# Optimization experiments

Hardware: AMD Instinct MI355X
Metric: run time of the kernel (lower is better)

Reference implementation:

```python
import jax, jax.numpy as jnp
import numpy as np

D_MODEL = 1024
NHEAD = 16
HEAD_DIM = D_MODEL // NHEAD
D_FF = 4096
EPS = 1e-5


def _layernorm(x, g, b):
    mu = jnp.mean(x, axis=-1, keepdims=True)
    var = jnp.mean((x - mu) ** 2, axis=-1, keepdims=True)
    return (x - mu) * jax.lax.rsqrt(var + EPS) * g + b


def setup_inputs() -> dict:
    key = jax.random.key(0)
    ks = jax.random.split(key, 13)
    s = 1.0 / np.sqrt(D_MODEL)
    sf = 1.0 / np.sqrt(D_FF)
    # weights stored as [in, out] (transposed torch Linear)
    return {
        "src": jax.random.normal(ks[0], (4, 2048, D_MODEL), jnp.float32),
        "Wq": jax.random.uniform(ks[1], (D_MODEL, D_MODEL), jnp.float32, -s, s),
        "bq": jnp.zeros((D_MODEL,), jnp.float32),
        "Wk": jax.random.uniform(ks[2], (D_MODEL, D_MODEL), jnp.float32, -s, s),
        "bk": jnp.zeros((D_MODEL,), jnp.float32),
        "Wv": jax.random.uniform(ks[3], (D_MODEL, D_MODEL), jnp.float32, -s, s),
        "bv": jnp.zeros((D_MODEL,), jnp.float32),
        "Wo": jax.random.uniform(ks[4], (D_MODEL, D_MODEL), jnp.float32, -s, s),
        "bo": jnp.zeros((D_MODEL,), jnp.float32),
        "W1": jax.random.uniform(ks[5], (D_MODEL, D_FF), jnp.float32, -s, s),
        "b1": jnp.zeros((D_FF,), jnp.float32),
        "W2": jax.random.uniform(ks[6], (D_FF, D_MODEL), jnp.float32, -sf, sf),
        "b2": jnp.zeros((D_MODEL,), jnp.float32),
        "g1": jnp.ones((D_MODEL,), jnp.float32),
        "be1": jnp.zeros((D_MODEL,), jnp.float32),
        "g2": jnp.ones((D_MODEL,), jnp.float32),
        "be2": jnp.zeros((D_MODEL,), jnp.float32),
    }


def reference(src, Wq, bq, Wk, bk, Wv, bv, Wo, bo, W1, b1, W2, b2, g1, be1, g2, be2):
    B, S, _ = src.shape
    scale = 1.0 / np.sqrt(HEAD_DIM)
    # project and split heads: [B, H, S, Dh]
    def heads(W, b):
        return (src @ W + b).reshape(B, S, NHEAD, HEAD_DIM).transpose(0, 2, 1, 3)
    Q, K, V = heads(Wq, bq), heads(Wk, bk), heads(Wv, bv)
    scores = jnp.einsum('bhqd,bhkd->bhqk', Q, K) * scale
    attn = jax.nn.softmax(scores, axis=-1)
    ctx = jnp.einsum('bhqk,bhkd->bhqd', attn, V)
    ctx = ctx.transpose(0, 2, 1, 3).reshape(B, S, D_MODEL)
    attn_out = ctx @ Wo + bo
    x = _layernorm(src + attn_out, g1, be1)
    ff = jax.nn.relu(x @ W1 + b1) @ W2 + b2
    return _layernorm(x + ff, g2, be2)
```

## Files before the change

kernel.cpp:

```cpp
#include <hip/hip_runtime.h>

typedef __attribute__((ext_vector_type(8))) short bf16x8;
typedef __attribute__((ext_vector_type(4))) float f32x4;
typedef unsigned short u16;
typedef unsigned int u32;

__device__ __forceinline__ u16 f2b(float f) {
  u32 u = __float_as_uint(f);
  u = (u + 0x7fffu + ((u >> 16) & 1u)) >> 16;
  return (u16)u;
}
__device__ __forceinline__ float b2f(u16 b) {
  return __uint_as_float(((u32)b) << 16);
}
__device__ __forceinline__ u32 cvtpk_bf16(float lo, float hi) {
  u32 r;
  asm("v_cvt_pk_bf16_f32 %0, %1, %2" : "=v"(r) : "v"(lo), "v"(hi));
  return r;
}
__device__ __forceinline__ void gload_lds16(const u16* g, u16* l) {
  __builtin_amdgcn_global_load_lds(
      (const __attribute__((address_space(1))) void*)g,
      (__attribute__((address_space(3))) void*)l, 16, 0, 0);
}

__global__ __launch_bounds__(256) void cvt_bf16(const float* __restrict__ in,
                                                u16* __restrict__ out, int n4) {
  int i = blockIdx.x * 256 + threadIdx.x;
  if (i >= n4) return;
  float4 v = ((const float4*)in)[i];
  ushort4 o;
  o.x = f2b(v.x); o.y = f2b(v.y); o.z = f2b(v.z); o.w = f2b(v.w);
  ((ushort4*)out)[i] = o;
}

__global__ __launch_bounds__(256) void transpose_w(const float* __restrict__ in,
                                                   u16* __restrict__ out,
                                                   int R, int C) {
  __shared__ float t[32][33];
  int tid = threadIdx.x, tx = tid & 31, ty = tid >> 5;
  int rb = blockIdx.y * 32, cb = blockIdx.x * 32;
  for (int i = 0; i < 4; i++)
    t[ty + i * 8][tx] = in[(size_t)(rb + ty + i * 8) * C + cb + tx];
  __syncthreads();
  for (int i = 0; i < 4; i++)
    out[(size_t)(cb + ty + i * 8) * R + rb + tx] = f2b(t[tx][ty + i * 8]);
}

__global__ __launch_bounds__(256) void concat3(const float* __restrict__ a,
                                               const float* __restrict__ b,
                                               const float* __restrict__ c,
                                               float* __restrict__ o) {
  int i = blockIdx.x * 256 + threadIdx.x;
  if (i >= 3072) return;
  o[i] = i < 1024 ? a[i] : (i < 2048 ? b[i - 1024] : c[i - 2048]);
}

__device__ __forceinline__ void stage_quarter(const u16* __restrict__ src,
                                              size_t rowbase, int K, int kcol,
                                              u16* dst, int c, int srow, int sg,
                                              int wid) {
  int row_ = c * 64 + srow;
  int gs_ = sg ^ (row_ & 7);
  gload_lds16(src + (rowbase + row_) * K + kcol + gs_ * 8,
              &dst[(c * 64 + wid * 8) * 64]);
}

template <bool PF>
__device__ __forceinline__ void tile_step(
    const u16* sAc, const u16* sBc, u16* sAn, u16* sBn,
    const u16* __restrict__ A, const u16* __restrict__ Bt, size_t abase,
    size_t bbase, int K, int Tn, int wm, int wn, int l16, int lq, int srow,
    int sg, int wid, f32x4 (&acc)[8][4]) {
  __syncthreads();
#pragma unroll
  for (int ks = 0; ks < 2; ++ks) {
    bf16x8 Bf[4], Af[4];
#pragma unroll
    for (int j = 0; j < 4; ++j) {
      int r = wn * 64 + j * 16 + l16;
      Bf[j] = *(const bf16x8*)&sBc[r * 64 + (((ks * 4 + lq) ^ (r & 7)) << 3)];
    }
#pragma unroll
    for (int i = 0; i < 4; ++i) {
      int r = wm * 128 + i * 16 + l16;
      Af[i] = *(const bf16x8*)&sAc[r * 64 + (((ks * 4 + lq) ^ (r & 7)) << 3)];
    }
    if (PF) {
      const u16* src = (ks == 0) ? A : Bt;
      size_t rb = (ks == 0) ? abase : bbase;
      u16* dst = (ks == 0) ? sAn : sBn;
      stage_quarter(src, rb, K, Tn * 64, dst, 0, srow, sg, wid);
      stage_quarter(src, rb, K, Tn * 64, dst, 1, srow, sg, wid);
    }
    __builtin_amdgcn_s_setprio(1);
#pragma unroll
    for (int i = 0; i < 4; ++i)
#pragma unroll
      for (int j = 0; j < 4; ++j)
        acc[i][j] = __builtin_amdgcn_mfma_f32_16x16x32_bf16(Af[i], Bf[j],
                                                            acc[i][j], 0, 0, 0);
    __builtin_amdgcn_s_setprio(0);
#pragma unroll
    for (int i = 0; i < 4; ++i) {
      int r = wm * 128 + 64 + i * 16 + l16;
      Af[i] = *(const bf16x8*)&sAc[r * 64 + (((ks * 4 + lq) ^ (r & 7)) << 3)];
    }
    if (PF) {
      const u16* src = (ks == 0) ? A : Bt;
      size_t rb = (ks == 0) ? abase : bbase;
      u16* dst = (ks == 0) ? sAn : sBn;
      stage_quarter(src, rb, K, Tn * 64, dst, 2, srow, sg, wid);
      stage_quarter(src, rb, K, Tn * 64, dst, 3, srow, sg, wid);
    }
    __builtin_amdgcn_s_setprio(1);
#pragma unroll
    for (int i = 0; i < 4; ++i)
#pragma unroll
      for (int j = 0; j < 4; ++j)
        acc[4 + i][j] = __builtin_amdgcn_mfma_f32_16x16x32_bf16(
            Af[i], Bf[j], acc[4 + i][j], 0, 0, 0);
    __builtin_amdgcn_s_setprio(0);
  }
}

template <int MODE>
__global__ __launch_bounds__(512, 1) void gemm256(const u16* __restrict__ A,
                                                  const u16* __restrict__ Bt,
                                                  const float* __restrict__ bias,
                                                  void* __restrict__ out,
                                                  int M, int N, int K,
                                                  float oscale) {
  __shared__ u16 sA0[256 * 64];
  __shared__ u16 sB0[256 * 64];
  __shared__ u16 sA1[256 * 64];
  __shared__ u16 sB1[256 * 64];
  const int tid = threadIdx.x, lane = tid & 63, wid = tid >> 6;
  const int l16 = lane & 15, lq = lane >> 4;
  const int wm = wid >> 2, wn = wid & 3;
  const size_t abase = (size_t)blockIdx.x * 256;
  const size_t bbase = (size_t)blockIdx.y * 256;
  const int srow = tid >> 3;
  const int sg = tid & 7;
  const int nt = K >> 6;

  f32x4 acc[8][4];
#pragma unroll
  for (int i = 0; i < 8; ++i)
#pragma unroll
    for (int j = 0; j < 4; ++j) acc[i][j] = (f32x4){0.f, 0.f, 0.f, 0.f};

#pragma unroll
  for (int c = 0; c < 4; ++c) {
    stage_quarter(A, abase, K, 0, sA0, c, srow, sg, wid);
    stage_quarter(Bt, bbase, K, 0, sB0, c, srow, sg, wid);
  }

  int T = 0;
  for (; T + 2 < nt; T += 2) {
    tile_step<true>(sA0, sB0, sA1, sB1, A, Bt, abase, bbase, K, T + 1, wm, wn,
                    l16, lq, srow, sg, wid, acc);
    tile_step<true>(sA1, sB1, sA0, sB0, A, Bt, abase, bbase, K, T + 2, wm, wn,
                    l16, lq, srow, sg, wid, acc);
  }
  tile_step<true>(sA0, sB0, sA1, sB1, A, Bt, abase, bbase, K, nt - 1, wm, wn,
                  l16, lq, srow, sg, wid, acc);
  tile_step<false>(sA1, sB1, sA0, sB0, A, Bt, abase, bbase, K, 0, wm, wn, l16,
                   lq, srow, sg, wid, acc);

  const int gmb = blockIdx.x * 256 + wm * 128;
  const int gnb = blockIdx.y * 256 + wn * 64;
#pragma unroll
  for (int i = 0; i < 8; ++i) {
    int gm0 = gmb + i * 16 + lq * 4;
#pragma unroll
    for (int j = 0; j < 4; ++j) {
      int gn = gnb + j * 16 + l16;
      float bv = bias[gn];
#pragma unroll
      for (int r = 0; r < 4; ++r) {
        float v = acc[i][j][r] + bv;
        ((u16*)out)[(size_t)(gm0 + r) * N + gn] = f2b(v > 0.f ? v : 0.f);
      }
    }
  }
}

template <bool PF>
__device__ __forceinline__ void tile_stepR(
    const u16* sAc, const u16* sBc, u16* sAn, u16* sBn,
    const u16* __restrict__ A, const u16* __restrict__ Bt, size_t abase,
    size_t bbase, int K, int Tn, int wm, int wn, int l16, int lq, int srow,
    int sg, int wid, f32x4 (&acc)[4][4]) {
  __syncthreads();
#pragma unroll
  for (int ks = 0; ks < 2; ++ks) {
    bf16x8 Bf[4], Af[4];
#pragma unroll
    for (int j = 0; j < 4; ++j) {
      int r = wn * 64 + j * 16 + l16;
      Bf[j] = *(const bf16x8*)&sBc[r * 64 + (((ks * 4 + lq) ^ (r & 7)) << 3)];
    }
#pragma unroll
    for (int i = 0; i < 4; ++i) {
      int r = wm * 64 + i * 16 + l16;
      Af[i] = *(const bf16x8*)&sAc[r * 64 + (((ks * 4 + lq) ^ (r & 7)) << 3)];
    }
    if (PF) {
      if (ks == 0) {
        stage_quarter(A, abase, K, Tn * 64, sAn, 0, srow, sg, wid);
        stage_quarter(A, abase, K, Tn * 64, sAn, 1, srow, sg, wid);
        stage_quarter(Bt, bbase, K, Tn * 64, sBn, 0, srow, sg, wid);
      } else {
        stage_quarter(Bt, bbase, K, Tn * 64, sBn, 1, srow, sg, wid);
        stage_quarter(Bt, bbase, K, Tn * 64, sBn, 2, srow, sg, wid);
        stage_quarter(Bt, bbase, K, Tn * 64, sBn, 3, srow, sg, wid);
      }
    }
    __builtin_amdgcn_s_setprio(1);
#pragma unroll
    for (int i = 0; i < 4; ++i)
#pragma unroll
      for (int j = 0; j < 4; ++j)
        acc[i][j] = __builtin_amdgcn_mfma_f32_16x16x32_bf16(Af[i], Bf[j],
                                                            acc[i][j], 0, 0, 0);
    __builtin_amdgcn_s_setprio(0);
  }
}

template <int MODE>
__global__ __launch_bounds__(512, 1) void gemmR(const u16* __restrict__ A,
                                                const u16* __restrict__ Bt,
                                                const float* __restrict__ bias,
                                                void* __restrict__ out,
                                                int M, int N, int K,
                                                float oscale) {
  __shared__ u16 sA0[128 * 64];
  __shared__ u16 sB0[256 * 64];
  __shared__ u16 sA1[128 * 64];
  __shared__ u16 sB1[256 * 64];
  const int tid = threadIdx.x, lane = tid & 63, wid = tid >> 6;
  const int l16 = lane & 15, lq = lane >> 4;
  const int wm = wid >> 2, wn = wid & 3;
  const size_t abase = (size_t)blockIdx.x * 128;
  const size_t bbase = (size_t)blockIdx.y * 256;
  const int srow = tid >> 3;
  const int sg = tid & 7;
  const int nt = K >> 6;

  f32x4 acc[4][4];
#pragma unroll
  for (int i = 0; i < 4; ++i)
#pragma unroll
    for (int j = 0; j < 4; ++j) acc[i][j] = (f32x4){0.f, 0.f, 0.f, 0.f};

#pragma unroll
  for (int c = 0; c < 2; ++c) stage_quarter(A, abase, K, 0, sA0, c, srow, sg, wid);
#pragma unroll
  for (int c = 0; c < 4; ++c) stage_quarter(Bt, bbase, K, 0, sB0, c, srow, sg, wid);

  int T = 0;
  for (; T + 2 < nt; T += 2) {
    tile_stepR<true>(sA0, sB0, sA1, sB1, A, Bt, abase, bbase, K, T + 1, wm, wn,
                     l16, lq, srow, sg, wid, acc);
    tile_stepR<true>(sA1, sB1, sA0, sB0, A, Bt, abase, bbase, K, T + 2, wm, wn,
                     l16, lq, srow, sg, wid, acc);
  }
  tile_stepR<true>(sA0, sB0, sA1, sB1, A, Bt, abase, bbase, K, nt - 1, wm, wn,
                   l16, lq, srow, sg, wid, acc);
  tile_stepR<false>(sA1, sB1, sA0, sB0, A, Bt, abase, bbase, K, 0, wm, wn, l16,
                    lq, srow, sg, wid, acc);

  const int gmb = blockIdx.x * 128 + wm * 64;
  const int gnb = blockIdx.y * 256 + wn * 64;
#pragma unroll
  for (int i = 0; i < 4; ++i) {
    int gm0 = gmb + i * 16 + lq * 4;
#pragma unroll
    for (int j = 0; j < 4; ++j) {
      int gn = gnb + j * 16 + l16;
      float bv = bias[gn];
      if constexpr (MODE == 1) {
#pragma unroll
        for (int r = 0; r < 4; ++r)
          ((u16*)out)[(size_t)(gm0 + r) * N + gn] = f2b(acc[i][j][r] + bv);
      } else {
        int sel = gn >> 10;
        int h = (gn & 1023) >> 6, d = gn & 63;
        int b = gm0 >> 11, s = gm0 & 2047;
        u16* o = (u16*)out + (size_t)sel * (8u << 20);
        if (sel == 2) {
          ushort4 w;
          w.x = f2b(acc[i][j][0] + bv);
          w.y = f2b(acc[i][j][1] + bv);
          w.z = f2b(acc[i][j][2] + bv);
          w.w = f2b(acc[i][j][3] + bv);
          *(ushort4*)(o + ((size_t)((b * 16 + h) * 64 + d)) * 2048 + s) = w;
        } else {
          float sc = (sel == 0) ? oscale : 1.f;
#pragma unroll
          for (int r = 0; r < 4; ++r)
            o[((size_t)(b * 16 + h) * 2048 + s + r) * 64 + d] =
                f2b((acc[i][j][r] + bv) * sc);
        }
      }
    }
  }
}

__global__ __launch_bounds__(512) void attn_fwd(const u16* __restrict__ Q,
                                                const u16* __restrict__ Kb,
                                                const u16* __restrict__ Vt,
                                                u16* __restrict__ ctx) {
  __shared__ u16 sK[64][64];
  __shared__ u16 sV[64][64];
  __shared__ u16 sP[8][16][72];
  const int tid = threadIdx.x, lane = tid & 63, wid = tid >> 6;
  const int l16 = lane & 15, lq = lane >> 4;
  const int bh = blockIdx.y, qt = blockIdx.x;
  const size_t base = (size_t)bh * (2048 * 64);
  const int xk = l16 & 7;

  bf16x8 qf[2];
  {
    int qrow = qt * 128 + wid * 16 + l16;
    qf[0] = *(const bf16x8*)(Q + base + (size_t)qrow * 64 + lq * 8);
    qf[1] = *(const bf16x8*)(Q + base + (size_t)qrow * 64 + 32 + lq * 8);
  }
  f32x4 o[4];
#pragma unroll
  for (int j = 0; j < 4; j++) o[j] = (f32x4){0.f, 0.f, 0.f, 0.f};
  float lrow = 0.f;

  const int srow = tid >> 3;
  const int sg8 = ((tid & 7) ^ (srow & 7)) * 8;
  const int wslot = (tid & 7) * 8;

  const u16* kp = Kb + base + (size_t)srow * 64 + sg8;
  const u16* vp = Vt + base + (size_t)srow * 2048 + sg8;

  uint4 rk = *(const uint4*)kp;
  uint4 rv = *(const uint4*)vp;

  for (int kv0 = 0; kv0 < 2048; kv0 += 64) {
    __syncthreads();
    *(uint4*)&sK[srow][wslot] = rk;
    *(uint4*)&sV[srow][wslot] = rv;
    if (kv0 + 64 < 2048) {
      int kn = kv0 + 64;
      rk = *(const uint4*)(kp + (size_t)kn * 64);
      rv = *(const uint4*)(vp + kn);
    }
    __syncthreads();

    f32x4 sf[4];
#pragma unroll
    for (int j = 0; j < 4; j++) sf[j] = (f32x4){0.f, 0.f, 0.f, 0.f};
    __builtin_amdgcn_s_setprio(1);
#pragma unroll
    for (int ks = 0; ks < 2; ks++)
#pragma unroll
      for (int j = 0; j < 4; j++) {
        bf16x8 kf = *(const bf16x8*)&sK[j * 16 + l16][((ks * 4 + lq) ^ xk) * 8];
        sf[j] = __builtin_amdgcn_mfma_f32_16x16x32_bf16(kf, qf[ks], sf[j], 0, 0, 0);
      }
    __builtin_amdgcn_s_setprio(0);

    float rs = 0.f;
#pragma unroll
    for (int j = 0; j < 4; j++) {
      float p0 = __builtin_amdgcn_exp2f(sf[j][0]);
      float p1 = __builtin_amdgcn_exp2f(sf[j][1]);
      float p2 = __builtin_amdgcn_exp2f(sf[j][2]);
      float p3 = __builtin_amdgcn_exp2f(sf[j][3]);
      rs += (p0 + p1) + (p2 + p3);
      uint2 w;
      w.x = cvtpk_bf16(p0, p1);
      w.y = cvtpk_bf16(p2, p3);
      *(uint2*)&sP[wid][l16][j * 16 + lq * 4] = w;
    }
    rs += __shfl_xor(rs, 16);
    rs += __shfl_xor(rs, 32);
    lrow += rs;

    __builtin_amdgcn_s_setprio(1);
#pragma unroll
    for (int ks = 0; ks < 2; ks++) {
      bf16x8 pf = *(const bf16x8*)&sP[wid][l16][ks * 32 + lq * 8];
#pragma unroll
      for (int j = 0; j < 4; j++) {
        bf16x8 vf = *(const bf16x8*)&sV[j * 16 + l16][((ks * 4 + lq) ^ xk) * 8];
        o[j] = __builtin_amdgcn_mfma_f32_16x16x32_bf16(pf, vf, o[j], 0, 0, 0);
      }
    }
    __builtin_amdgcn_s_setprio(0);
  }

  float lval[4];
#pragma unroll
  for (int r = 0; r < 4; r++) lval[r] = 1.f / __shfl(lrow, lq * 4 + r);
  const int b = bh >> 4, h = bh & 15;
#pragma unroll
  for (int j = 0; j < 4; j++)
#pragma unroll
    for (int r = 0; r < 4; r++) {
      int srw = qt * 128 + wid * 16 + lq * 4 + r;
      int d = j * 16 + l16;
      ctx[((size_t)(b * 2048 + srw)) * 1024 + h * 64 + d] = f2b(o[j][r] * lval[r]);
    }
}

template <int A_BF16, int B_BF16, int WRITE_F32>
__global__ __launch_bounds__(256) void ln_res(const void* __restrict__ a,
                                              const void* __restrict__ bsrc,
                                              const float* __restrict__ g,
                                              const float* __restrict__ be,
                                              float* __restrict__ outf,
                                              u16* __restrict__ outb) {
  const int row = blockIdx.x, tid = threadIdx.x;
  const size_t off = (size_t)row * 1024 + tid * 4;
  float4 x;
  if constexpr (A_BF16) {
    ushort4 av = *(const ushort4*)((const u16*)a + off);
    x.x = b2f(av.x); x.y = b2f(av.y); x.z = b2f(av.z); x.w = b2f(av.w);
  } else {
    x = *(const float4*)((const float*)a + off);
  }
  if constexpr (B_BF16) {
    ushort4 bv = *(const ushort4*)((const u16*)bsrc + off);
    x.x += b2f(bv.x); x.y += b2f(bv.y); x.z += b2f(bv.z); x.w += b2f(bv.w);
  } else {
    float4 bb = *(const float4*)((const float*)bsrc + off);
    x.x += bb.x; x.y += bb.y; x.z += bb.z; x.w += bb.w;
  }
  float s = x.x + x.y + x.z + x.w;
  float s2 = x.x * x.x + x.y * x.y + x.z * x.z + x.w * x.w;
  for (int o = 1; o < 64; o <<= 1) {
    s += __shfl_xor(s, o);
    s2 += __shfl_xor(s2, o);
  }
  __shared__ float rbuf[8];
  int lane = tid & 63, wid = tid >> 6;
  if (lane == 0) { rbuf[wid] = s; rbuf[4 + wid] = s2; }
  __syncthreads();
  s = rbuf[0] + rbuf[1] + rbuf[2] + rbuf[3];
  s2 = rbuf[4] + rbuf[5] + rbuf[6] + rbuf[7];
  float mu = s * (1.f / 1024.f);
  float var = s2 * (1.f / 1024.f) - mu * mu;
  float rstd = rsqrtf(var + 1e-5f);
  int c = tid * 4;
  float y0 = (x.x - mu) * rstd * g[c + 0] + be[c + 0];
  float y1 = (x.y - mu) * rstd * g[c + 1] + be[c + 1];
  float y2 = (x.z - mu) * rstd * g[c + 2] + be[c + 2];
  float y3 = (x.w - mu) * rstd * g[c + 3] + be[c + 3];
  if constexpr (WRITE_F32) {
    float4 y; y.x = y0; y.y = y1; y.z = y2; y.w = y3;
    *(float4*)(outf + off) = y;
  } else {
    ushort4 yb;
    yb.x = f2b(y0); yb.y = f2b(y1); yb.z = f2b(y2); yb.w = f2b(y3);
    *(ushort4*)(outb + off) = yb;
  }
}

extern "C" void kernel_launch(void* const* d_in, const int* in_sizes, int n_in,
                              void* d_out, int out_size, void* d_ws, size_t ws_size,
                              hipStream_t stream) {
  const float* src = (const float*)d_in[0];
  const float* Wq = (const float*)d_in[1];
  const float* bq = (const float*)d_in[2];
  const float* Wk = (const float*)d_in[3];
  const float* bk = (const float*)d_in[4];
  const float* Wv = (const float*)d_in[5];
  const float* bv = (const float*)d_in[6];
  const float* Wo = (const float*)d_in[7];
  const float* bo = (const float*)d_in[8];
  const float* W1 = (const float*)d_in[9];
  const float* b1 = (const float*)d_in[10];
  const float* W2 = (const float*)d_in[11];
  const float* b2 = (const float*)d_in[12];
  const float* g1 = (const float*)d_in[13];
  const float* be1 = (const float*)d_in[14];
  const float* g2 = (const float*)d_in[15];
  const float* be2 = (const float*)d_in[16];
  float* out = (float*)d_out;
  char* ws = (char*)d_ws;
  const size_t MB = 1ull << 20;

  u16* XB    = (u16*)(ws + 0);
  u16* WQKVT = (u16*)(ws + 16 * MB);
  u16* WOT   = (u16*)(ws + 22 * MB);
  u16* W1T   = (u16*)(ws + 24 * MB);
  u16* W2T   = (u16*)(ws + 32 * MB);
  float* bqkv = (float*)(ws + 40 * MB);
  u16* Qb    = (u16*)(ws + 41 * MB);
  u16* Kbuf  = (u16*)(ws + 57 * MB);
  u16* Vt    = (u16*)(ws + 73 * MB);
  u16* CTX   = XB;
  u16* AO    = (u16*)(ws + 41 * MB);
  u16* H1    = (u16*)(ws + 57 * MB);
  u16* XBUF  = (u16*)(ws + 121 * MB);
  u16* FF    = XB;

  const float QSCALE = 0.125f * 1.44269504088896340736f;

  cvt_bf16<<<dim3(8192), dim3(256), 0, stream>>>(src, XB, 2097152);
  transpose_w<<<dim3(32, 32), dim3(256), 0, stream>>>(Wq, WQKVT, 1024, 1024);
  transpose_w<<<dim3(32, 32), dim3(256), 0, stream>>>(Wk, WQKVT + 1024 * 1024, 1024, 1024);
  transpose_w<<<dim3(32, 32), dim3(256), 0, stream>>>(Wv, WQKVT + 2048 * 1024, 1024, 1024);
  transpose_w<<<dim3(32, 32), dim3(256), 0, stream>>>(Wo, WOT, 1024, 1024);
  transpose_w<<<dim3(128, 32), dim3(256), 0, stream>>>(W1, W1T, 1024, 4096);
  transpose_w<<<dim3(32, 128), dim3(256), 0, stream>>>(W2, W2T, 4096, 1024);
  concat3<<<dim3(12), dim3(256), 0, stream>>>(bq, bk, bv, bqkv);

  gemmR<6><<<dim3(64, 12), dim3(512), 0, stream>>>(XB, WQKVT, bqkv, Qb,
                                                   8192, 3072, 1024, QSCALE);
  attn_fwd<<<dim3(16, 64), dim3(512), 0, stream>>>(Qb, Kbuf, Vt, CTX);
  gemmR<1><<<dim3(64, 4), dim3(512), 0, stream>>>(CTX, WOT, bo, AO,
                                                  8192, 1024, 1024, 1.0f);
  ln_res<0, 1, 0><<<dim3(8192), dim3(256), 0, stream>>>(src, AO, g1, be1, nullptr, XBUF);
  gemm256<2><<<dim3(32, 16), dim3(512), 0, stream>>>(XBUF, W1T, b1, H1,
                                                     8192, 4096, 1024, 1.0f);
  gemmR<1><<<dim3(64, 4), dim3(512), 0, stream>>>(H1, W2T, b2, FF,
                                                  8192, 1024, 4096, 1.0f);
  ln_res<1, 1, 1><<<dim3(8192), dim3(256), 0, stream>>>(XBUF, FF, g2, be2, out, nullptr);
}
```

Baseline: 352.5 us.

## Fuse preprocessing kernels into one launch and defer softmax row-sum shuffles

Merges the input bf16 conversion, the six weight transpose launches and the bias concat into a single prep kernel that dispatches on block index, cutting seven launches and their inter-kernel gaps. The attention kernel also stops reducing the per-row softmax sum across lanes on every key tile. Each lane now accumulates a partial sum and the cross-lane shuffles run once after the loop. The prep kernel now mixes branches with different shared-memory use in one grid, and per-lane partial sums change the floating-point summation order slightly.

```diff
diff --git a/kernel.cpp b/kernel.cpp
--- a/kernel.cpp
+++ b/kernel.cpp
@@ -24,22 +24,12 @@
       (__attribute__((address_space(3))) void*)l, 16, 0, 0);
 }
 
-__global__ __launch_bounds__(256) void cvt_bf16(const float* __restrict__ in,
-                                                u16* __restrict__ out, int n4) {
-  int i = blockIdx.x * 256 + threadIdx.x;
-  if (i >= n4) return;
-  float4 v = ((const float4*)in)[i];
-  ushort4 o;
-  o.x = f2b(v.x); o.y = f2b(v.y); o.z = f2b(v.z); o.w = f2b(v.w);
-  ((ushort4*)out)[i] = o;
-}
-
-__global__ __launch_bounds__(256) void transpose_w(const float* __restrict__ in,
-                                                   u16* __restrict__ out,
-                                                   int R, int C) {
+__device__ __forceinline__ void tr_tile(const float* __restrict__ in,
+                                        u16* __restrict__ out, int R, int C,
+                                        int bx, int by, int tid) {
   __shared__ float t[32][33];
-  int tid = threadIdx.x, tx = tid & 31, ty = tid >> 5;
-  int rb = blockIdx.y * 32, cb = blockIdx.x * 32;
+  int tx = tid & 31, ty = tid >> 5;
+  int rb = by * 32, cb = bx * 32;
   for (int i = 0; i < 4; i++)
     t[ty + i * 8][tx] = in[(size_t)(rb + ty + i * 8) * C + cb + tx];
   __syncthreads();
@@ -47,13 +37,39 @@
     out[(size_t)(cb + ty + i * 8) * R + rb + tx] = f2b(t[tx][ty + i * 8]);
 }
 
-__global__ __launch_bounds__(256) void concat3(const float* __restrict__ a,
-                                               const float* __restrict__ b,
-                                               const float* __restrict__ c,
-                                               float* __restrict__ o) {
-  int i = blockIdx.x * 256 + threadIdx.x;
-  if (i >= 3072) return;
-  o[i] = i < 1024 ? a[i] : (i < 2048 ? b[i - 1024] : c[i - 2048]);
+__global__ __launch_bounds__(256) void prep(
+    const float* __restrict__ src, u16* __restrict__ XB,
+    const float* __restrict__ Wq, const float* __restrict__ Wk,
+    const float* __restrict__ Wv, const float* __restrict__ Wo,
+    const float* __restrict__ W1, const float* __restrict__ W2,
+    u16* __restrict__ WQKVT, u16* __restrict__ WOT, u16* __restrict__ W1T,
+    u16* __restrict__ W2T, const float* __restrict__ bq,
+    const float* __restrict__ bk, const float* __restrict__ bv,
+    float* __restrict__ bqkv) {
+  const int blk = blockIdx.x, tid = threadIdx.x;
+  if (blk < 8192) {
+    int i = blk * 256 + tid;
+    float4 v = ((const float4*)src)[i];
+    ushort4 o;
+    o.x = f2b(v.x); o.y = f2b(v.y); o.z = f2b(v.z); o.w = f2b(v.w);
+    ((ushort4*)XB)[i] = o;
+  } else if (blk < 8192 + 4096) {
+    int t = blk - 8192;
+    int w = t >> 10, tt = t & 1023;
+    const float* in = (w == 0) ? Wq : (w == 1) ? Wk : (w == 2) ? Wv : Wo;
+    u16* out = (w == 3) ? WOT : (WQKVT + (size_t)w * 1024 * 1024);
+    tr_tile(in, out, 1024, 1024, tt & 31, tt >> 5, tid);
+  } else if (blk < 8192 + 4096 + 4096) {
+    int t = blk - (8192 + 4096);
+    tr_tile(W1, W1T, 1024, 4096, t & 127, t >> 7, tid);
+  } else if (blk < 8192 + 4096 + 4096 + 4096) {
+    int t = blk - (8192 + 4096 + 4096);
+    tr_tile(W2, W2T, 4096, 1024, t & 31, t >> 5, tid);
+  } else {
+    int i = (blk - (8192 + 4096 + 4096 + 4096)) * 256 + tid;
+    if (i < 3072)
+      bqkv[i] = i < 1024 ? bq[i] : (i < 2048 ? bk[i - 1024] : bv[i - 2048]);
+  }
 }
 
 __device__ __forceinline__ void stage_quarter(const u16* __restrict__ src,
@@ -366,22 +382,18 @@
       }
     __builtin_amdgcn_s_setprio(0);
 
-    float rs = 0.f;
 #pragma unroll
     for (int j = 0; j < 4; j++) {
       float p0 = __builtin_amdgcn_exp2f(sf[j][0]);
       float p1 = __builtin_amdgcn_exp2f(sf[j][1]);
       float p2 = __builtin_amdgcn_exp2f(sf[j][2]);
       float p3 = __builtin_amdgcn_exp2f(sf[j][3]);
-      rs += (p0 + p1) + (p2 + p3);
+      lrow += (p0 + p1) + (p2 + p3);
       uint2 w;
       w.x = cvtpk_bf16(p0, p1);
       w.y = cvtpk_bf16(p2, p3);
       *(uint2*)&sP[wid][l16][j * 16 + lq * 4] = w;
     }
-    rs += __shfl_xor(rs, 16);
-    rs += __shfl_xor(rs, 32);
-    lrow += rs;
 
     __builtin_amdgcn_s_setprio(1);
 #pragma unroll
@@ -396,6 +408,8 @@
     __builtin_amdgcn_s_setprio(0);
   }
 
+  lrow += __shfl_xor(lrow, 16);
+  lrow += __shfl_xor(lrow, 32);
   float lval[4];
 #pragma unroll
   for (int r = 0; r < 4; r++) lval[r] = 1.f / __shfl(lrow, lq * 4 + r);
@@ -504,14 +518,8 @@
 
   const float QSCALE = 0.125f * 1.44269504088896340736f;
 
-  cvt_bf16<<<dim3(8192), dim3(256), 0, stream>>>(src, XB, 2097152);
-  transpose_w<<<dim3(32, 32), dim3(256), 0, stream>>>(Wq, WQKVT, 1024, 1024);
-  transpose_w<<<dim3(32, 32), dim3(256), 0, stream>>>(Wk, WQKVT + 1024 * 1024, 1024, 1024);
-  transpose_w<<<dim3(32, 32), dim3(256), 0, stream>>>(Wv, WQKVT + 2048 * 1024, 1024, 1024);
-  transpose_w<<<dim3(32, 32), dim3(256), 0, stream>>>(Wo, WOT, 1024, 1024);
-  transpose_w<<<dim3(128, 32), dim3(256), 0, stream>>>(W1, W1T, 1024, 4096);
-  transpose_w<<<dim3(32, 128), dim3(256), 0, stream>>>(W2, W2T, 4096, 1024);
-  concat3<<<dim3(12), dim3(256), 0, stream>>>(bq, bk, bv, bqkv);
+  prep<<<dim3(8192 + 4096 + 4096 + 4096 + 13), dim3(256), 0, stream>>>(
+      src, XB, Wq, Wk, Wv, Wo, W1, W2, WQKVT, WOT, W1T, W2T, bq, bk, bv, bqkv);
 
   gemmR<6><<<dim3(64, 12), dim3(512), 0, stream>>>(XB, WQKVT, bqkv, Qb,
                                                    8192, 3072, 1024, QSCALE);
```

New measurement: 338.9 us, median of 3. 1.04x faster.
